# Kernel tuning notes

Hardware: AMD Instinct MI355X
Metric: run time of the kernel (lower is better)

Reference implementation:

```python
import math
import jax, jax.numpy as jnp
import numpy as np

D_MODEL = 1024
NUM_HEADS = 16
D_K = D_MODEL // NUM_HEADS
RANK = 16
B, L = 2, 2048


def setup_inputs() -> dict:
    key = jax.random.key(0)
    ks = jax.random.split(key, 10)
    w_scale = 0.02  # keep activations well-scaled like trained linears
    return {
        "x_q": jax.random.normal(ks[0], (B, L, D_MODEL), jnp.float32),
        "x_kv": jax.random.normal(ks[1], (B, L, D_MODEL), jnp.float32),
        "Wq": jax.random.normal(ks[2], (D_MODEL, D_MODEL), jnp.float32) * w_scale,
        "bq": jnp.zeros((D_MODEL,), jnp.float32),
        "Wk": jax.random.normal(ks[3], (D_MODEL, D_MODEL), jnp.float32) * w_scale,
        "bk": jnp.zeros((D_MODEL,), jnp.float32),
        "Wv": jax.random.normal(ks[4], (D_MODEL, D_MODEL), jnp.float32) * w_scale,
        "bv": jnp.zeros((D_MODEL,), jnp.float32),
        "Wo": jax.random.normal(ks[5], (D_MODEL, D_MODEL), jnp.float32) * w_scale,
        "bo": jnp.zeros((D_MODEL,), jnp.float32),
        "U_bil": jax.random.normal(ks[6], (NUM_HEADS, D_K, RANK), jnp.float32) * 0.02,
        "V_bil": jax.random.normal(ks[7], (NUM_HEADS, D_K, RANK), jnp.float32) * 0.02,
        "padding_mask": jnp.zeros((B, L), bool),  # True = padded KV position
    }


def reference(x_q, x_kv, Wq, bq, Wk, bk, Wv, bv, Wo, bo, U_bil, V_bil, padding_mask):
    b, l, _ = x_q.shape
    # torch nn.Linear: y = x @ W.T + b
    Q = (x_q @ Wq.T + bq).reshape(b, l, NUM_HEADS, D_K).transpose(0, 2, 1, 3)  # [B,H,L,dk]
    K = (x_kv @ Wk.T + bk).reshape(b, l, NUM_HEADS, D_K).transpose(0, 2, 1, 3)
    V = (x_kv @ Wv.T + bv).reshape(b, l, NUM_HEADS, D_K).transpose(0, 2, 1, 3)
    # low-rank bilinear projections: [B,H,L,rank]
    Q_proj = jnp.einsum("bhld,hdr->bhlr", Q, U_bil)
    K_proj = jnp.einsum("bhld,hdr->bhlr", K, V_bil)
    scores = jnp.einsum("bhqr,bhkr->bhqk", Q_proj, K_proj) / math.sqrt(RANK)  # [B,H,L,L]
    scores = jnp.where(padding_mask[:, None, None, :], jnp.float32(-10000.0), scores)
    attn = jax.nn.softmax(scores, axis=-1)  # dropout is identity in eval mode
    ctx = jnp.einsum("bhqk,bhkd->bhqd", attn, V)
    ctx = ctx.transpose(0, 2, 1, 3).reshape(b, l, D_MODEL)
    return ctx @ Wo.T + bo
```

## Files before the change

### kernel.cpp

```cpp
#include <hip/hip_runtime.h>
#include <hip/hip_bf16.h>

#define DM   1024
#define NH   16
#define DK   64
#define RK   16
#define BB   2
#define LL   2048
#define TT   (BB*LL)
#define NSPL 2


typedef float f4   __attribute__((ext_vector_type(4)));
typedef float f16v __attribute__((ext_vector_type(16)));
typedef short s8v  __attribute__((ext_vector_type(8)));
typedef unsigned int u2v __attribute__((ext_vector_type(2)));
typedef unsigned int u4v __attribute__((ext_vector_type(4)));

static __device__ __forceinline__ unsigned short f2b(float f) {
  __hip_bfloat16 h = __float2bfloat16(f);
  unsigned short u;
  __builtin_memcpy(&u, &h, 2);
  return u;
}
static __device__ __forceinline__ float b2f(unsigned short u) {
  __hip_bfloat16 h;
  __builtin_memcpy(&h, &u, 2);
  return __bfloat162float(h);
}

static __device__ __forceinline__ void gld_lds16(const void* g, void* l) {
  __builtin_amdgcn_global_load_lds(
      (const __attribute__((address_space(1))) unsigned int*)g,
      (__attribute__((address_space(3))) unsigned int*)l, 16, 0, 0);
}

static __device__ __forceinline__ void wait_vm0_barrier() {
  asm volatile("s_waitcnt vmcnt(0)" ::: "memory");
  __builtin_amdgcn_s_barrier();
}

static __device__ __forceinline__ void cast_rng(
    const float* __restrict__ s, unsigned short* __restrict__ d,
    int n4, int lb, int nb, int tid) {
  for (int i = lb*256 + tid; i < n4; i += nb*256) {
    const float4 v = ((const float4*)s)[i];
    ushort4 o;
    o.x = f2b(v.x); o.y = f2b(v.y); o.z = f2b(v.z); o.w = f2b(v.w);
    ((ushort4*)d)[i] = o;
  }
}

__global__ __launch_bounds__(256) void prep_k(
    const float* __restrict__ xq,  const float* __restrict__ xkv,
    const float* __restrict__ Wv,  const float* __restrict__ Wo,
    unsigned short* __restrict__ xq_b,  unsigned short* __restrict__ xkv_b,
    unsigned short* __restrict__ Wv_b,  unsigned short* __restrict__ Wo_b,
    const float* __restrict__ Wq,  const float* __restrict__ Wk,
    const float* __restrict__ Uq,  const float* __restrict__ Uk,
    unsigned short* __restrict__ Aq, unsigned short* __restrict__ Ak,
    const float* __restrict__ bq,  const float* __restrict__ bk,
    float* __restrict__ bpq, float* __restrict__ bpk) {
  __shared__ float sh[64*16 + 4*64];
  const int x = blockIdx.x, tid = threadIdx.x;
  if (x < 1024) {
    cast_rng(xq,  xq_b,  TT*DM/4, x,        1024, tid);
  } else if (x < 2048) {
    cast_rng(xkv, xkv_b, TT*DM/4, x - 1024, 1024, tid);
  } else if (x < 2304) {
    cast_rng(Wv,  Wv_b,  DM*DM/4, x - 2048, 256, tid);
  } else if (x < 2560) {
    cast_rng(Wo,  Wo_b,  DM*DM/4, x - 2304, 256, tid);
  } else if (x < 3072) {
    const int fidx = x - 2560;
    const int sel = fidx >> 8, f = fidx & 255;
    const float* W = sel ? Wk : Wq;
    const float* U = sel ? Uk : Uq;
    unsigned short* At = sel ? Ak : Aq;
    const int i0 = (f & 15) * 64, h = f >> 4;
    float* Us = sh;
    float* Ws = sh + 1024;
    const int il = tid & 63, rr = tid >> 6;
    for (int t = tid; t < 64*16; t += 256)
      Us[t] = U[(size_t)(h*DK + (t >> 4))*RK + (t & 15)];
    float acc[4] = {};
    for (int d0 = 0; d0 < DK; d0 += 4) {
      __syncthreads();
      Ws[rr*64 + il] = W[(size_t)(h*DK + d0 + rr)*DM + i0 + il];
      __syncthreads();
#pragma unroll
      for (int dd = 0; dd < 4; ++dd) {
        const float w = Ws[dd*64 + il];
#pragma unroll
        for (int j = 0; j < 4; ++j)
          acc[j] += w * Us[(d0 + dd)*16 + rr*4 + j];
      }
    }
#pragma unroll
    for (int j = 0; j < 4; ++j)
      At[(size_t)(h*RK + rr*4 + j)*DM + i0 + il] = f2b(acc[j]);
  } else {
    const int h = tid >> 4, r = tid & 15;
    float aq = 0.f, ak = 0.f;
    for (int d = 0; d < DK; ++d) {
      aq += bq[h*DK + d] * Uq[(size_t)(h*DK + d)*RK + r];
      ak += bk[h*DK + d] * Uk[(size_t)(h*DK + d)*RK + r];
    }
    bpq[tid] = aq; bpk[tid] = ak;
  }
}

__global__ __launch_bounds__(256) void proj_k(
    const unsigned short* __restrict__ xq_b, const unsigned short* __restrict__ xkv_b,
    const unsigned short* __restrict__ Atq,  const unsigned short* __restrict__ Atk,
    const float* __restrict__ bpq, const float* __restrict__ bpk,
    unsigned short* __restrict__ Qp, unsigned short* __restrict__ Kp,
    const unsigned short* __restrict__ Wv_b, const float* __restrict__ bv,
    unsigned short* __restrict__ Vt) {
  __shared__ __align__(16) unsigned short shm[16384];
  const int f = blockIdx.x, tid = threadIdx.x;
  const int wave = tid >> 6, lane = tid & 63;
  const int quad = lane >> 4, l15 = lane & 15;
  const int ar = tid >> 2, ac = (tid & 3) * 8;
  const f4 z = {0.f, 0.f, 0.f, 0.f};

  if (f < 256) {
    const int xb = f & 63, yb = (f >> 6) & 1, zb = f >> 7;
    const unsigned short* Ag = zb ? xkv_b : xq_b;
    const unsigned short* Bg = zb ? Atk : Atq;
    const float* bias = zb ? bpk : bpq;
    unsigned short* C = zb ? Kp : Qp;
    unsigned short* Xs = shm;
    unsigned short* Bq = shm + 4096;
    const int t0 = xb*64, n0 = yb*128, nh = wave*32;
    f4 acc[4][2];
#pragma unroll
    for (int a = 0; a < 4; ++a) { acc[a][0] = z; acc[a][1] = z; }

    auto STAGE = [&](int buf, int k0) {
      gld_lds16(&Ag[(size_t)(t0 + ar)*DM + k0 + ac],      &Xs[buf*2048 + wave*512]);
      gld_lds16(&Bg[(size_t)(n0 + ar)*DM + k0 + ac],      &Bq[buf*4096 + wave*512]);
      gld_lds16(&Bg[(size_t)(n0 + 64 + ar)*DM + k0 + ac], &Bq[buf*4096 + 2048 + wave*512]);
    };
    STAGE(0, 0);
    wait_vm0_barrier();
    int cur = 0;
    for (int k0 = 0; k0 < DM; k0 += 32) {
      if (k0 + 32 < DM) STAGE(cur ^ 1, k0 + 32);
      s8v af[4], bf[2];
#pragma unroll
      for (int ms = 0; ms < 4; ++ms)
        af[ms] = *(const s8v*)&Xs[cur*2048 + (ms*16 + l15)*32 + quad*8];
#pragma unroll
      for (int ns = 0; ns < 2; ++ns)
        bf[ns] = *(const s8v*)&Bq[cur*4096 + (nh + ns*16 + l15)*32 + quad*8];
#pragma unroll
      for (int ms = 0; ms < 4; ++ms)
#pragma unroll
        for (int ns = 0; ns < 2; ++ns)
          acc[ms][ns] = __builtin_amdgcn_mfma_f32_16x16x32_bf16(
              af[ms], bf[ns], acc[ms][ns], 0, 0, 0);
      wait_vm0_barrier();
      cur ^= 1;
    }
#pragma unroll
    for (int ms = 0; ms < 4; ++ms) {
      const int tb = t0 + ms*16 + quad*4;
#pragma unroll
      for (int ns = 0; ns < 2; ++ns) {
        const int o = n0 + nh + ns*16 + l15;
        const float bvv = bias[o];
        f4 a = acc[ms][ns];
#pragma unroll
        for (int rg = 0; rg < 4; ++rg) {
          const int tt = tb + rg;
          C[(((size_t)(tt >> 11)*NH + (o >> 4))*LL + (tt & 2047))*RK + (o & 15)]
              = f2b(a[rg] + bvv);
        }
      }
    }
  } else {
    const int g = f - 256, gx = g & 31, gy = g >> 5;
    unsigned short* As = shm;
    unsigned short* Bs = shm + 8192;
    const int t0 = gx*128, n0 = gy*128;
    f4 acc[2][8];
#pragma unroll
    for (int m = 0; m < 2; ++m)
#pragma unroll
      for (int n = 0; n < 8; ++n) acc[m][n] = z;

    auto STAGE = [&](int buf, int k0) {
      gld_lds16(&xkv_b[(size_t)(t0 + ar)*DM + k0 + ac],      &As[buf*4096 + wave*512]);
      gld_lds16(&xkv_b[(size_t)(t0 + 64 + ar)*DM + k0 + ac], &As[buf*4096 + 2048 + wave*512]);
      gld_lds16(&Wv_b[(size_t)(n0 + ar)*DM + k0 + ac],       &Bs[buf*4096 + wave*512]);
      gld_lds16(&Wv_b[(size_t)(n0 + 64 + ar)*DM + k0 + ac],  &Bs[buf*4096 + 2048 + wave*512]);
    };
    STAGE(0, 0);
    wait_vm0_barrier();
    int cur = 0;
    for (int k0 = 0; k0 < DM; k0 += 32) {
      if (k0 + 32 < DM) STAGE(cur ^ 1, k0 + 32);
      s8v af[2], bf[8];
#pragma unroll
      for (int ms = 0; ms < 2; ++ms)
        af[ms] = *(const s8v*)&As[cur*4096 + (wave*32 + ms*16 + l15)*32 + quad*8];
#pragma unroll
      for (int ns = 0; ns < 8; ++ns)
        bf[ns] = *(const s8v*)&Bs[cur*4096 + (ns*16 + l15)*32 + quad*8];
#pragma unroll
      for (int ms = 0; ms < 2; ++ms)
#pragma unroll
        for (int ns = 0; ns < 8; ++ns)
          acc[ms][ns] = __builtin_amdgcn_mfma_f32_16x16x32_bf16(
              af[ms], bf[ns], acc[ms][ns], 0, 0, 0);
      wait_vm0_barrier();
      cur ^= 1;
    }
#pragma unroll
    for (int ms = 0; ms < 2; ++ms) {
      const int tb = t0 + wave*32 + ms*16 + quad*4;
#pragma unroll
      for (int ns = 0; ns < 8; ++ns) {
        const int o = n0 + ns*16 + l15;
        const float bvv = bv[o];
        f4 a = acc[ms][ns];
        const int bb = tb >> 11, l = tb & 2047;
        ushort4 pk;
        pk.x = f2b(a[0] + bvv); pk.y = f2b(a[1] + bvv);
        pk.z = f2b(a[2] + bvv); pk.w = f2b(a[3] + bvv);
        *(ushort4*)&Vt[((size_t)bb*DM + o)*LL + l] = pk;
      }
    }
  }
}

template<bool MASKED>
static __device__ __forceinline__ void softmax_pack(
    const f16v& s0, const f16v& s1, const unsigned long long mb, const int hi,
    float& den, unsigned int (&Pd)[2][4][2]) {
#pragma unroll
  for (int nt = 0; nt < 2; ++nt) {
    const f16v& sv = nt ? s1 : s0;
#pragma unroll
    for (int r = 0; r < 4; ++r) {
      float ep[4];
#pragma unroll
      for (int j = 0; j < 4; ++j) {
        float em = __expf(sv[r*4 + j] * 0.25f);
        if (MASKED) {
          const int kloc = nt*32 + j + 8*r + 4*hi;
          if ((mb >> kloc) & 1ull) em = 0.f;
        }
        den += em;
        ep[j] = em - 1.f;
      }
      asm("v_cvt_pk_bf16_f32 %0, %1, %2"
          : "=v"(Pd[nt][r][0]) : "v"(ep[0]), "v"(ep[1]));
      asm("v_cvt_pk_bf16_f32 %0, %1, %2"
          : "=v"(Pd[nt][r][1]) : "v"(ep[2]), "v"(ep[3]));
    }
  }
}

__global__ __launch_bounds__(256) void attn_k(
    const unsigned short* __restrict__ Qp, const unsigned short* __restrict__ Kp,
    const unsigned short* __restrict__ Vt,
    const unsigned char* __restrict__ msk,
    unsigned short* __restrict__ P, float* __restrict__ denP,
    float* __restrict__ Vsum) {
  __shared__ __align__(16) unsigned short Ks[2][2][64][8];
  __shared__ __align__(16) unsigned short Vs[2][8][64][8];
  const int tid = threadIdx.x;

  if (blockIdx.z == 4) {
    if (blockIdx.y >= BB) return;
    const int h = blockIdx.x, b = blockIdx.y;
    const int d = tid >> 2, part = tid & 3;
    const unsigned short* row = Vt + ((size_t)b*DM + h*DK + d)*LL + part*512;
    float s = 0.f;
    for (int i = 0; i < 512; i += 8) {
      const s8v v = *(const s8v*)&row[i];
#pragma unroll
      for (int j = 0; j < 8; ++j) s += b2f((unsigned short)v[j]);
    }
    s += __shfl_xor(s, 1);
    s += __shfl_xor(s, 2);
    if (part == 0) Vsum[((size_t)b*NH + h)*DK + d] = s;
    return;
  }

  const int q0 = blockIdx.x * 128, h = blockIdx.y;
  const int b = blockIdx.z & (BB - 1), ksp = blockIdx.z >> 1;
  const int kbeg = ksp * (LL / NSPL);
  const int NT = (LL / NSPL) / 64;
  const int w = tid >> 6, lane = tid & 63;
  const int l31 = lane & 31, hi = lane >> 5;

  const s8v qfrag = *(const s8v*)&Qp[
      (((size_t)b*NH + h)*LL + q0 + w*32 + l31)*RK + hi*8];

  const int sr = tid >> 2, sp = tid & 3;
  const unsigned short* __restrict__ Vrow =
      Vt + ((size_t)b*DM + h*DK + sr)*LL + kbeg;
  const unsigned short* __restrict__ Kbase =
      Kp + (((size_t)b*NH + h)*LL + kbeg + sr)*RK + sp*4;
  const unsigned char*  __restrict__ Mrow = msk + (size_t)b*LL + kbeg + lane;

  u2v kpre; s8v vpre0, vpre1;
  unsigned char mcur, mnext;

  kpre  = *(const u2v*)&Kbase[0];
  vpre0 = *(const s8v*)&Vrow[sp*16];
  vpre1 = *(const s8v*)&Vrow[sp*16 + 8];
  mcur  = Mrow[0];
  *(u2v*)&Ks[0][sp>>1][sr][(sp&1)*4] = kpre;
  *(s8v*)&Vs[0][sp*2][sr][0]   = vpre0;
  *(s8v*)&Vs[0][sp*2+1][sr][0] = vpre1;
  kpre  = *(const u2v*)&Kbase[(size_t)64*RK];
  vpre0 = *(const s8v*)&Vrow[64 + sp*16];
  vpre1 = *(const s8v*)&Vrow[64 + sp*16 + 8];
  mnext = Mrow[64];
  __syncthreads();

  f16v acc0, acc1, z16;
#pragma unroll
  for (int i = 0; i < 16; ++i) { acc0[i] = 0.f; acc1[i] = 0.f; z16[i] = 0.f; }
  float den = 0.f;

  for (int t = 0; t < NT; ++t) {
    const int cur = t & 1;
    const unsigned long long mb = __ballot(mcur != 0);

    const s8v kf0 = *(const s8v*)&Ks[cur][hi][l31][0];
    const s8v kf1 = *(const s8v*)&Ks[cur][hi][32 + l31][0];

    const f16v s0 = __builtin_amdgcn_mfma_f32_32x32x16_bf16(kf0, qfrag, z16, 0, 0, 0);
    const f16v s1 = __builtin_amdgcn_mfma_f32_32x32x16_bf16(kf1, qfrag, z16, 0, 0, 0);

    unsigned int Pd[2][4][2];
    if (__builtin_expect(mb != 0ull, 0))
      softmax_pack<true >(s0, s1, mb, hi, den, Pd);
    else
      softmax_pack<false>(s0, s1, mb, hi, den, Pd);

#pragma unroll
    for (int kc = 0; kc < 4; ++kc) {
      const int nt = kc >> 1, a = (kc & 1)*2;
      const u2v r0 = __builtin_amdgcn_permlane32_swap(
          Pd[nt][a][0], Pd[nt][a+1][0], false, false);
      const u2v r1 = __builtin_amdgcn_permlane32_swap(
          Pd[nt][a][1], Pd[nt][a+1][1], false, false);
      u4v efi;
      efi[0] = r0[0];
      efi[1] = r1[0];
      efi[2] = r0[1];
      efi[3] = r1[1];
      const s8v ef = __builtin_bit_cast(s8v, efi);
      const s8v vf0 = *(const s8v*)&Vs[cur][kc*2 + hi][l31][0];
      const s8v vf1 = *(const s8v*)&Vs[cur][kc*2 + hi][32 + l31][0];
      acc0 = __builtin_amdgcn_mfma_f32_32x32x16_bf16(ef, vf0, acc0, 0, 0, 0);
      acc1 = __builtin_amdgcn_mfma_f32_32x32x16_bf16(ef, vf1, acc1, 0, 0, 0);
    }

    if (t + 1 < NT) {
      *(u2v*)&Ks[cur^1][sp>>1][sr][(sp&1)*4] = kpre;
      *(s8v*)&Vs[cur^1][sp*2][sr][0]   = vpre0;
      *(s8v*)&Vs[cur^1][sp*2+1][sr][0] = vpre1;
      const int tn = (t + 2 < NT) ? t + 2 : NT - 1;
      kpre  = *(const u2v*)&Kbase[(size_t)tn*64*RK];
      vpre0 = *(const s8v*)&Vrow[tn*64 + sp*16];
      vpre1 = *(const s8v*)&Vrow[tn*64 + sp*16 + 8];
      mcur  = mnext;
      mnext = Mrow[tn*64];
    }
    __syncthreads();
  }

  den += __shfl_xor(den, 32);
  if (hi == 0)
    denP[(((size_t)ksp*BB + b)*NH + h)*LL + q0 + w*32 + l31] = den;

#pragma unroll
  for (int rg = 0; rg < 16; ++rg) {
    const int qr = (rg & 3) + 8*(rg >> 2) + 4*hi;
    const size_t pbase =
        ((size_t)ksp*TT + b*LL + q0 + w*32 + qr)*DM + h*DK;
    P[pbase + l31]      = f2b(acc0[rg]);
    P[pbase + 32 + l31] = f2b(acc1[rg]);
  }
}

__global__ __launch_bounds__(256) void outred_k(
    const unsigned short* __restrict__ P, const float* __restrict__ Vsum,
    const float* __restrict__ denP, const unsigned short* __restrict__ Bg,
    const float* __restrict__ bias, float* __restrict__ C) {
  __shared__ __align__(16) unsigned short P0s[2][2048];
  __shared__ __align__(16) unsigned short P1s[2][2048];
  __shared__ __align__(16) unsigned short Bs[2][4096];
  __shared__ float vsS[1024];
  __shared__ float invS[64][16];
  const int f = blockIdx.x;
  const int t0 = (f & 63) * 64, n0 = (f >> 6) * 128;
  const int tid = threadIdx.x, wave = tid >> 6, lane = tid & 63;
  const int quad = lane >> 4, l15 = lane & 15;
  const int nh = wave * 32;
  const int ar = tid >> 2, ac = (tid & 3) * 8;
  const int trow = t0 + ar;
  const int b = t0 >> 11;

  for (int i = tid; i < 1024; i += 256)
    vsS[i] = Vsum[(size_t)b*DM + i];
  {
    const int r = tid >> 2, h0 = (tid & 3) * 4;
    const int lr = (t0 + r) & 2047;
#pragma unroll
    for (int j = 0; j < 4; ++j) {
      const int h = h0 + j;
      const float dn = denP[((size_t)b*NH + h)*LL + lr] +
                       denP[(((size_t)BB + b)*NH + h)*LL + lr];
      invS[r][h] = 1.f / fmaxf(dn, 1e-30f);
    }
  }

  auto STAGE = [&](int buf, int k0) {
    gld_lds16(&P[(size_t)trow*DM + k0 + ac],             &P0s[buf][wave*512]);
    gld_lds16(&P[((size_t)TT + trow)*DM + k0 + ac],      &P1s[buf][wave*512]);
    gld_lds16(&Bg[(size_t)(n0 + ar)*DM + k0 + ac],       &Bs[buf][wave*512]);
    gld_lds16(&Bg[(size_t)(n0 + 64 + ar)*DM + k0 + ac],  &Bs[buf][2048 + wave*512]);
  };
  STAGE(0, 0);
  asm volatile("s_waitcnt vmcnt(0) lgkmcnt(0)" ::: "memory");
  __builtin_amdgcn_s_barrier();

  const f4 z = {0.f, 0.f, 0.f, 0.f};
  f4 acc[4][2];
#pragma unroll
  for (int a = 0; a < 4; ++a) { acc[a][0] = z; acc[a][1] = z; }

  int cur = 0;
  for (int k0 = 0; k0 < DM; k0 += 32) {
    if (k0 + 32 < DM) STAGE(cur ^ 1, k0 + 32);
    const int hk = k0 >> 6;
    const f4 vq0 = *(const f4*)&vsS[k0 + quad*8];
    const f4 vq1 = *(const f4*)&vsS[k0 + quad*8 + 4];
    s8v af[4], bf[2];
#pragma unroll
    for (int ms = 0; ms < 4; ++ms) {
      const int r16 = ms*16 + l15;
      const float inv = invS[r16][hk];
      const s8v p0 = *(const s8v*)&P0s[cur][r16*32 + quad*8];
      const s8v p1 = *(const s8v*)&P1s[cur][r16*32 + quad*8];
      float e[8];
#pragma unroll
      for (int j = 0; j < 4; ++j) {
        e[j]     = (vq0[j] + b2f((unsigned short)p0[j])
                           + b2f((unsigned short)p1[j])) * inv;
        e[4 + j] = (vq1[j] + b2f((unsigned short)p0[4+j])
                           + b2f((unsigned short)p1[4+j])) * inv;
      }
      unsigned int d0, d1, d2, d3;
      asm("v_cvt_pk_bf16_f32 %0, %1, %2" : "=v"(d0) : "v"(e[0]), "v"(e[1]));
      asm("v_cvt_pk_bf16_f32 %0, %1, %2" : "=v"(d1) : "v"(e[2]), "v"(e[3]));
      asm("v_cvt_pk_bf16_f32 %0, %1, %2" : "=v"(d2) : "v"(e[4]), "v"(e[5]));
      asm("v_cvt_pk_bf16_f32 %0, %1, %2" : "=v"(d3) : "v"(e[6]), "v"(e[7]));
      u4v efi; efi[0] = d0; efi[1] = d1; efi[2] = d2; efi[3] = d3;
      af[ms] = __builtin_bit_cast(s8v, efi);
    }
#pragma unroll
    for (int ns = 0; ns < 2; ++ns)
      bf[ns] = *(const s8v*)&Bs[cur][(nh + ns*16 + l15)*32 + quad*8];
#pragma unroll
    for (int ms = 0; ms < 4; ++ms)
#pragma unroll
      for (int ns = 0; ns < 2; ++ns)
        acc[ms][ns] = __builtin_amdgcn_mfma_f32_16x16x32_bf16(
            af[ms], bf[ns], acc[ms][ns], 0, 0, 0);
    wait_vm0_barrier();
    cur ^= 1;
  }

#pragma unroll
  for (int ms = 0; ms < 4; ++ms) {
    const int tb = t0 + ms*16 + quad*4;
#pragma unroll
    for (int ns = 0; ns < 2; ++ns) {
      const int o = n0 + nh + ns*16 + l15;
      const float bv = bias[o];
      f4 a = acc[ms][ns];
#pragma unroll
      for (int rg = 0; rg < 4; ++rg)
        C[(size_t)(tb + rg)*DM + o] = a[rg] + bv;
    }
  }
}

extern "C" void kernel_launch(void* const* d_in, const int* in_sizes, int n_in,
                              void* d_out, int out_size, void* d_ws, size_t ws_size,
                              hipStream_t stream) {
  (void)in_sizes; (void)n_in; (void)out_size; (void)ws_size;
  const float* x_q   = (const float*)d_in[0];
  const float* x_kv  = (const float*)d_in[1];
  const float* Wq    = (const float*)d_in[2];
  const float* bq    = (const float*)d_in[3];
  const float* Wk    = (const float*)d_in[4];
  const float* bk    = (const float*)d_in[5];
  const float* Wv    = (const float*)d_in[6];
  const float* bv    = (const float*)d_in[7];
  const float* Wo    = (const float*)d_in[8];
  const float* bo    = (const float*)d_in[9];
  const float* U_bil = (const float*)d_in[10];
  const float* V_bil = (const float*)d_in[11];
  const unsigned char* pmask = (const unsigned char*)d_in[12];
  float* out = (float*)d_out;

  char* w = (char*)d_ws;
  unsigned short* xq_b  = (unsigned short*)(w);
  unsigned short* xkv_b = (unsigned short*)(w +  8388608);
  unsigned short* Wv_b  = (unsigned short*)(w + 16777216);
  unsigned short* Wo_b  = (unsigned short*)(w + 18874368);
  unsigned short* Atq   = (unsigned short*)(w + 20971520);
  unsigned short* Atk   = (unsigned short*)(w + 21495808);
  float*          bpq   = (float*)(w + 22020096);
  float*          bpk   = (float*)(w + 22021120);
  unsigned short* Qp    = (unsigned short*)(w + 22022144);
  unsigned short* Kp    = (unsigned short*)(w + 24119296);
  unsigned short* Vt    = (unsigned short*)(w + 26216448);
  float*          Vsum  = (float*)(w + 34605056);
  float*          denP  = (float*)(w + 34613248);
  unsigned short* Pbuf  = (unsigned short*)w;

  prep_k<<<3073, 256, 0, stream>>>(
      x_q, x_kv, Wv, Wo, xq_b, xkv_b, Wv_b, Wo_b,
      Wq, Wk, U_bil, V_bil, Atq, Atk, bq, bk, bpq, bpk);
  proj_k<<<512, 256, 0, stream>>>(
      xq_b, xkv_b, Atq, Atk, bpq, bpk, Qp, Kp, Wv_b, bv, Vt);
  attn_k<<<dim3(LL/128, NH, 5), 256, 0, stream>>>(
      Qp, Kp, Vt, pmask, Pbuf, denP, Vsum);
  outred_k<<<512, 256, 0, stream>>>(Pbuf, Vsum, denP, Wo_b, bo, out);
}
```

Baseline: 229.4 us.

## Fold softmax scale into Q projection and pack exp-minus-one with packed adds

Folds the 1/sqrt(rank) score scale into the precomputed Q-side projection weights and bias, which removes a multiply per score in the attention inner loop. The denominator is now accumulated from (exp-1) values using packed v_pk_add_f32, and the missing constant is added back at the end. The K and V LDS tiles are padded from 64 to 65 rows to reduce bank conflicts, and attn_k gets an occupancy hint in its launch bounds. Scaling before the bf16 rounding of the projection weights slightly changes numerics, and accumulating exp-1 can lose a little precision in the denominator.

New measurement: 227.3 us. No clear change (-0.9%).

```diff
diff --git a/kernel.cpp b/kernel.cpp
--- a/kernel.cpp
+++ b/kernel.cpp
@@ -12,6 +12,7 @@
 
 
 typedef float f4   __attribute__((ext_vector_type(4)));
+typedef float f2   __attribute__((ext_vector_type(2)));
 typedef float f16v __attribute__((ext_vector_type(16)));
 typedef short s8v  __attribute__((ext_vector_type(8)));
 typedef unsigned int u2v __attribute__((ext_vector_type(2)));
@@ -77,6 +78,7 @@
     const float* W = sel ? Wk : Wq;
     const float* U = sel ? Uk : Uq;
     unsigned short* At = sel ? Ak : Aq;
+    const float qs = sel ? 1.f : 0.25f;
     const int i0 = (f & 15) * 64, h = f >> 4;
     float* Us = sh;
     float* Ws = sh + 1024;
@@ -98,7 +100,7 @@
     }
 #pragma unroll
     for (int j = 0; j < 4; ++j)
-      At[(size_t)(h*RK + rr*4 + j)*DM + i0 + il] = f2b(acc[j]);
+      At[(size_t)(h*RK + rr*4 + j)*DM + i0 + il] = f2b(acc[j] * qs);
   } else {
     const int h = tid >> 4, r = tid & 15;
     float aq = 0.f, ak = 0.f;
@@ -106,7 +108,7 @@
       aq += bq[h*DK + d] * Uq[(size_t)(h*DK + d)*RK + r];
       ak += bk[h*DK + d] * Uk[(size_t)(h*DK + d)*RK + r];
     }
-    bpq[tid] = aq; bpk[tid] = ak;
+    bpq[tid] = aq * 0.25f; bpk[tid] = ak;
   }
 }
 
@@ -238,39 +240,41 @@
 template<bool MASKED>
 static __device__ __forceinline__ void softmax_pack(
     const f16v& s0, const f16v& s1, const unsigned long long mb, const int hi,
-    float& den, unsigned int (&Pd)[2][4][2]) {
+    f2& den2, unsigned int (&Pd)[2][4][2]) {
+  const f2 neg1 = {-1.f, -1.f};
 #pragma unroll
   for (int nt = 0; nt < 2; ++nt) {
     const f16v& sv = nt ? s1 : s0;
 #pragma unroll
     for (int r = 0; r < 4; ++r) {
-      float ep[4];
-#pragma unroll
-      for (int j = 0; j < 4; ++j) {
-        float em = __expf(sv[r*4 + j] * 0.25f);
+#pragma unroll
+      for (int jp = 0; jp < 2; ++jp) {
+        f2 em2;
+        em2[0] = __expf(sv[r*4 + jp*2]);
+        em2[1] = __expf(sv[r*4 + jp*2 + 1]);
         if (MASKED) {
-          const int kloc = nt*32 + j + 8*r + 4*hi;
-          if ((mb >> kloc) & 1ull) em = 0.f;
+          const int kl = nt*32 + jp*2 + 8*r + 4*hi;
+          if ((mb >> kl) & 1ull)       em2[0] = 0.f;
+          if ((mb >> (kl + 1)) & 1ull) em2[1] = 0.f;
         }
-        den += em;
-        ep[j] = em - 1.f;
+        f2 ep2;
+        asm("v_pk_add_f32 %0, %1, %2" : "=v"(ep2) : "v"(em2), "v"(neg1));
+        asm("v_pk_add_f32 %0, %0, %1" : "+v"(den2) : "v"(ep2));
+        asm("v_cvt_pk_bf16_f32 %0, %1, %2"
+            : "=v"(Pd[nt][r][jp]) : "v"(ep2[0]), "v"(ep2[1]));
       }
-      asm("v_cvt_pk_bf16_f32 %0, %1, %2"
-          : "=v"(Pd[nt][r][0]) : "v"(ep[0]), "v"(ep[1]));
-      asm("v_cvt_pk_bf16_f32 %0, %1, %2"
-          : "=v"(Pd[nt][r][1]) : "v"(ep[2]), "v"(ep[3]));
-    }
-  }
-}
-
-__global__ __launch_bounds__(256) void attn_k(
+    }
+  }
+}
+
+__global__ __launch_bounds__(256, 4) void attn_k(
     const unsigned short* __restrict__ Qp, const unsigned short* __restrict__ Kp,
     const unsigned short* __restrict__ Vt,
     const unsigned char* __restrict__ msk,
     unsigned short* __restrict__ P, float* __restrict__ denP,
     float* __restrict__ Vsum) {
-  __shared__ __align__(16) unsigned short Ks[2][2][64][8];
-  __shared__ __align__(16) unsigned short Vs[2][8][64][8];
+  __shared__ __align__(16) unsigned short Ks[2][2][65][8];
+  __shared__ __align__(16) unsigned short Vs[2][8][65][8];
   const int tid = threadIdx.x;
 
   if (blockIdx.z == 4) {
@@ -326,7 +330,7 @@
   f16v acc0, acc1, z16;
 #pragma unroll
   for (int i = 0; i < 16; ++i) { acc0[i] = 0.f; acc1[i] = 0.f; z16[i] = 0.f; }
-  float den = 0.f;
+  f2 den2 = {0.f, 0.f};
 
   for (int t = 0; t < NT; ++t) {
     const int cur = t & 1;
@@ -340,9 +344,9 @@
 
     unsigned int Pd[2][4][2];
     if (__builtin_expect(mb != 0ull, 0))
-      softmax_pack<true >(s0, s1, mb, hi, den, Pd);
+      softmax_pack<true >(s0, s1, mb, hi, den2, Pd);
     else
-      softmax_pack<false>(s0, s1, mb, hi, den, Pd);
+      softmax_pack<false>(s0, s1, mb, hi, den2, Pd);
 
 #pragma unroll
     for (int kc = 0; kc < 4; ++kc) {
@@ -377,6 +381,7 @@
     __syncthreads();
   }
 
+  float den = den2[0] + den2[1] + (float)(32 * NT);
   den += __shfl_xor(den, 32);
   if (hi == 0)
     denP[(((size_t)ksp*BB + b)*NH + h)*LL + q0 + w*32 + l31] = den;
```
